# Performance work log

Hardware: AMD Instinct MI355X
Metric: run time of the kernel (lower is better)

Reference implementation:

```python
import jax, jax.numpy as jnp
import numpy as np

TAU = 24            # highpass cutoff period (init kwarg tau)
B, L, D = 16, 4096, 512


def _butter_hp2(tau):
    """2nd-order Butterworth highpass biquad via bilinear transform.
    Matches scipy.signal.iirfilter(2, 1/tau, btype='highpass', output='sos',
    ftype='butter', fs=2.0): one SOS section.
    Returns b: [1,3] numerator taps, A: [1,2,2] companion matrix
    [[-a1,-a2],[1,0]] exactly as built in IIRDecompositionLayer.__init__."""
    K = np.tan(np.pi / (2.0 * tau))  # tan(pi*Wn/2), Wn = 1/tau (Nyquist=1)
    norm = 1.0 / (1.0 + np.sqrt(2.0) * K + K * K)
    b = np.array([norm, -2.0 * norm, norm], dtype=np.float32)
    a1 = 2.0 * (K * K - 1.0) * norm
    a2 = (1.0 - np.sqrt(2.0) * K + K * K) * norm
    A = np.array([[-a1, -a2], [1.0, 0.0]], dtype=np.float32)
    return b[None, :], A[None, :, :]


def setup_inputs() -> dict:
    key = jax.random.key(0)
    x = jax.random.normal(key, (B, L, D), dtype=jnp.float32)
    b, A = _butter_hp2(TAU)
    return {"x": x, "b_coef": jnp.asarray(b), "a_mat": jnp.asarray(A)}


def _combine(c_prev, c_next):
    # composition of affine maps s -> A s + u (linear recurrence)
    A1, u1 = c_prev
    A2, u2 = c_next
    return (jnp.matmul(A2, A1), jnp.einsum('lsn,lbnd->lbsd', A2, u1) + u2)


def _section_pass(x, b3, A, reverse):
    # x: [B,L,D]; b3: [3]; A: [2,2]
    Lx = x.shape[1]
    if reverse:
        # anti-causal taps with 'edge' padding: x[min(t+i, L-1)]
        x1 = jnp.concatenate([x[:, 1:], x[:, -1:]], axis=1)
        x2 = jnp.concatenate([x[:, 2:], x[:, -1:], x[:, -1:]], axis=1)
    else:
        # causal taps with 'edge' padding: x[max(t-i, 0)]
        x1 = jnp.concatenate([x[:, :1], x[:, :-1]], axis=1)
        x2 = jnp.concatenate([x[:, :1], x[:, :1], x[:, :-2]], axis=1)
    bx = b3[0] * x + b3[1] * x1 + b3[2] * x2          # [B,L,D]
    u = jnp.stack([bx, jnp.zeros_like(bx)], axis=2)   # [B,L,2,D] state drive
    u = jnp.transpose(u, (1, 0, 2, 3))                # [L,B,2,D]
    # 'edge' initial state: s_init = [bx_edge, bx_edge], folded into u at the
    # first scanned element (index 0 forward, L-1 reverse)
    idx = Lx - 1 if reverse else 0
    c = bx[:, idx]                                    # [B,D]
    carry = jnp.stack([c, c], axis=1)                 # [B,2,D]
    u = u.at[idx].add(jnp.einsum('sn,bnd->bsd', A, carry))
    As = jnp.broadcast_to(A, (Lx, 2, 2))
    _, res = jax.lax.associative_scan(_combine, (As, u), reverse=reverse)
    return jnp.transpose(res[:, :, 0, :], (1, 0, 2))  # output = state[0] -> [B,L,D]


def reference(x, b_coef, a_mat):
    y = x
    n_sections = b_coef.shape[0]
    for s in range(n_sections):            # small fixed cascade
        for rev in (False, True):          # filtfilt: forward then backward
            y = _section_pass(y, b_coef[s], a_mat[s], rev)
    seasonality = y
    trend = x - seasonality
    return (seasonality, trend)
```

## Files before the change

kernel.cpp:

```cpp
#include <hip/hip_runtime.h>

#define B_   16
#define L_   4096
#define D_   512
#define C_   32
#define NC_  128
#define LOG2C_ 5


__device__ __forceinline__ void pow_M(float A00, float A01,
                                      float& m00, float& m01,
                                      float& m10, float& m11) {
  m00 = A00; m01 = A01; m10 = 1.f; m11 = 0.f;
#pragma unroll
  for (int it = 0; it < LOG2C_; ++it) {
    float n00 = m00 * m00 + m01 * m10;
    float n01 = m00 * m01 + m01 * m11;
    float n10 = m10 * m00 + m11 * m10;
    float n11 = m10 * m01 + m11 * m11;
    m00 = n00; m01 = n01; m10 = n10; m11 = n11;
  }
}

__global__ __launch_bounds__(256) void k_fwd_part(const float* __restrict__ x,
                                                  const float* __restrict__ bc,
                                                  const float* __restrict__ am,
                                                  float* __restrict__ p) {
  int g = blockIdx.x * 256 + threadIdx.x;
  int d = g % D_;
  int i = (g / D_) % NC_;
  int b = g / (D_ * NC_);
  float b0 = bc[0], b1 = bc[1], b2 = bc[2];
  float A00 = am[0], A01 = am[1];
  const float* xb = x + (size_t)b * L_ * D_ + d;
  int l0 = i * C_;
  float xm1, xm2;
  if (i == 0) {
    xm1 = xm2 = xb[0];
  } else {
    xm1 = xb[(size_t)(l0 - 1) * D_];
    xm2 = xb[(size_t)(l0 - 2) * D_];
  }
  float y1 = 0.f, y2 = 0.f;
#pragma unroll
  for (int t = 0; t < C_; ++t) {
    float cur = xb[(size_t)(l0 + t) * D_];
    float bx = b0 * cur + b1 * xm1 + b2 * xm2;
    float y = bx + A00 * y1 + A01 * y2;
    xm2 = xm1; xm1 = cur;
    y2 = y1; y1 = y;
  }
  float* pp = p + (size_t)(b * NC_ + i) * 2 * D_ + d;
  pp[0]  = y1;
  pp[D_] = y2;
}

__global__ __launch_bounds__(256) void k_fwd_scan(const float* __restrict__ x,
                                                  const float* __restrict__ bc,
                                                  const float* __restrict__ am,
                                                  const float* __restrict__ p,
                                                  float* __restrict__ sf) {
  int g = blockIdx.x * 256 + threadIdx.x;
  int d = g % D_;
  int b = g / D_;
  float b0 = bc[0], b1 = bc[1], b2 = bc[2];
  float A00 = am[0], A01 = am[1];
  float m00, m01, m10, m11;
  pow_M(A00, A01, m00, m01, m10, m11);

  float x0 = x[(size_t)b * L_ * D_ + d];
  float bx0 = (b0 + b1 + b2) * x0;
  float s0 = bx0, s1 = bx0;
  const float* pp = p + (size_t)b * NC_ * 2 * D_ + d;
  float* sfp = sf + (size_t)b * (NC_ + 1) * 2 * D_ + d;
  sfp[0] = s0;
  sfp[D_] = s1;
  for (int i = 0; i < NC_; ++i) {
    float p0 = pp[(size_t)i * 2 * D_];
    float p1 = pp[(size_t)i * 2 * D_ + D_];
    float n0 = m00 * s0 + m01 * s1 + p0;
    float n1 = m10 * s0 + m11 * s1 + p1;
    s0 = n0; s1 = n1;
    sfp[(size_t)(i + 1) * 2 * D_]      = s0;
    sfp[(size_t)(i + 1) * 2 * D_ + D_] = s1;
  }
}

__global__ __launch_bounds__(256) void k_bwd_part(const float* __restrict__ x,
                                                  const float* __restrict__ bc,
                                                  const float* __restrict__ am,
                                                  const float* __restrict__ sf,
                                                  float* __restrict__ q) {
  int g = blockIdx.x * 256 + threadIdx.x;
  int d = g % D_;
  int i = (g / D_) % NC_;
  int b = g / (D_ * NC_);
  float b0 = bc[0], b1 = bc[1], b2 = bc[2];
  float A00 = am[0], A01 = am[1];
  const float* xb = x + (size_t)b * L_ * D_ + d;
  const float* sfp = sf + (size_t)b * (NC_ + 1) * 2 * D_ + (size_t)i * 2 * D_ + d;
  float y1 = sfp[0];
  float y2 = sfp[D_];
  int l0 = i * C_;
  float xm1, xm2;
  if (i == 0) {
    xm1 = xm2 = xb[0];
  } else {
    xm1 = xb[(size_t)(l0 - 1) * D_];
    xm2 = xb[(size_t)(l0 - 2) * D_];
  }
  float f[C_];
#pragma unroll
  for (int t = 0; t < C_; ++t) {
    float cur = xb[(size_t)(l0 + t) * D_];
    float bx = b0 * cur + b1 * xm1 + b2 * xm2;
    float y = bx + A00 * y1 + A01 * y2;
    f[t] = y;
    xm2 = xm1; xm1 = cur;
    y2 = y1; y1 = y;
  }
  float fe0, fe1;
  if (i < NC_ - 1) {
    float cur = xb[(size_t)(l0 + C_) * D_];
    float bx = b0 * cur + b1 * xm1 + b2 * xm2;
    fe0 = bx + A00 * y1 + A01 * y2;
    xm2 = xm1; xm1 = cur; y2 = y1; y1 = fe0;
    cur = xb[(size_t)(l0 + C_ + 1) * D_];
    bx = b0 * cur + b1 * xm1 + b2 * xm2;
    fe1 = bx + A00 * y1 + A01 * y2;
  } else {
    fe0 = f[C_ - 1];
    fe1 = f[C_ - 1];
  }
  float z1 = 0.f, z2 = 0.f;
#pragma unroll
  for (int t = C_ - 1; t >= 0; --t) {
    float fp1 = (t == C_ - 1) ? fe0 : f[t + 1];
    float fp2 = (t == C_ - 1) ? fe1 : ((t == C_ - 2) ? fe0 : f[t + 2]);
    float bxb = b0 * f[t] + b1 * fp1 + b2 * fp2;
    float z = bxb + A00 * z1 + A01 * z2;
    z2 = z1; z1 = z;
  }
  float* qp = q + (size_t)(b * NC_ + i) * 2 * D_ + d;
  qp[0]  = z1;
  qp[D_] = z2;
}

__global__ __launch_bounds__(256) void k_bwd_scan(const float* __restrict__ bc,
                                                  const float* __restrict__ am,
                                                  const float* __restrict__ sf,
                                                  const float* __restrict__ q,
                                                  float* __restrict__ sb) {
  int g = blockIdx.x * 256 + threadIdx.x;
  int d = g % D_;
  int b = g / D_;
  float b0 = bc[0], b1 = bc[1], b2 = bc[2];
  float A00 = am[0], A01 = am[1];
  float m00, m01, m10, m11;
  pow_M(A00, A01, m00, m01, m10, m11);

  float fL1 = sf[(size_t)b * (NC_ + 1) * 2 * D_ + (size_t)NC_ * 2 * D_ + d];
  float c = (b0 + b1 + b2) * fL1;
  float s0 = c, s1 = c;
  const float* qp = q + (size_t)b * NC_ * 2 * D_ + d;
  float* sbp = sb + (size_t)b * NC_ * 2 * D_ + d;
  sbp[(size_t)(NC_ - 1) * 2 * D_]      = s0;
  sbp[(size_t)(NC_ - 1) * 2 * D_ + D_] = s1;
  for (int i = NC_ - 1; i >= 1; --i) {
    float q0 = qp[(size_t)i * 2 * D_];
    float q1 = qp[(size_t)i * 2 * D_ + D_];
    float n0 = m00 * s0 + m01 * s1 + q0;
    float n1 = m10 * s0 + m11 * s1 + q1;
    s0 = n0; s1 = n1;
    sbp[(size_t)(i - 1) * 2 * D_]      = s0;
    sbp[(size_t)(i - 1) * 2 * D_ + D_] = s1;
  }
}

__global__ __launch_bounds__(256) void k_final(const float* __restrict__ x,
                                               const float* __restrict__ bc,
                                               const float* __restrict__ am,
                                               const float* __restrict__ sf,
                                               const float* __restrict__ sb,
                                               float* __restrict__ seas,
                                               float* __restrict__ trend) {
  int g = blockIdx.x * 256 + threadIdx.x;
  int d = g % D_;
  int i = (g / D_) % NC_;
  int b = g / (D_ * NC_);
  float b0 = bc[0], b1 = bc[1], b2 = bc[2];
  float A00 = am[0], A01 = am[1];
  const float* xb = x + (size_t)b * L_ * D_ + d;
  const float* sfp = sf + (size_t)b * (NC_ + 1) * 2 * D_ + (size_t)i * 2 * D_ + d;
  float y1 = sfp[0];
  float y2 = sfp[D_];
  int l0 = i * C_;
  float xm1, xm2;
  if (i == 0) {
    xm1 = xm2 = xb[0];
  } else {
    xm1 = xb[(size_t)(l0 - 1) * D_];
    xm2 = xb[(size_t)(l0 - 2) * D_];
  }
  float f[C_];
  float xa[C_];
#pragma unroll
  for (int t = 0; t < C_; ++t) {
    float cur = xb[(size_t)(l0 + t) * D_];
    xa[t] = cur;
    float bx = b0 * cur + b1 * xm1 + b2 * xm2;
    float y = bx + A00 * y1 + A01 * y2;
    f[t] = y;
    xm2 = xm1; xm1 = cur;
    y2 = y1; y1 = y;
  }
  float fe0, fe1;
  if (i < NC_ - 1) {
    float cur = xb[(size_t)(l0 + C_) * D_];
    float bx = b0 * cur + b1 * xm1 + b2 * xm2;
    fe0 = bx + A00 * y1 + A01 * y2;
    xm2 = xm1; xm1 = cur; y2 = y1; y1 = fe0;
    cur = xb[(size_t)(l0 + C_ + 1) * D_];
    bx = b0 * cur + b1 * xm1 + b2 * xm2;
    fe1 = bx + A00 * y1 + A01 * y2;
  } else {
    fe0 = f[C_ - 1];
    fe1 = f[C_ - 1];
  }
  const float* sbp = sb + (size_t)b * NC_ * 2 * D_ + (size_t)i * 2 * D_ + d;
  float z1 = sbp[0];
  float z2 = sbp[D_];
  float* sp = seas + (size_t)b * L_ * D_ + d;
  float* tp = trend + (size_t)b * L_ * D_ + d;
#pragma unroll
  for (int t = C_ - 1; t >= 0; --t) {
    float fp1 = (t == C_ - 1) ? fe0 : f[t + 1];
    float fp2 = (t == C_ - 1) ? fe1 : ((t == C_ - 2) ? fe0 : f[t + 2]);
    float bxb = b0 * f[t] + b1 * fp1 + b2 * fp2;
    float yb = bxb + A00 * z1 + A01 * z2;
    size_t o = (size_t)(l0 + t) * D_;
    __builtin_nontemporal_store(yb, sp + o);
    __builtin_nontemporal_store(xa[t] - yb, tp + o);
    z2 = z1; z1 = yb;
  }
}

extern "C" void kernel_launch(void* const* d_in, const int* in_sizes, int n_in,
                              void* d_out, int out_size, void* d_ws, size_t ws_size,
                              hipStream_t stream) {
  const float* x  = (const float*)d_in[0];
  const float* bc = (const float*)d_in[1];
  const float* am = (const float*)d_in[2];
  float* out = (float*)d_out;
  float* seas  = out;
  float* trend = out + (size_t)B_ * L_ * D_;

  float* ws = (float*)d_ws;
  size_t PN  = (size_t)B_ * NC_ * 2 * D_;
  size_t SFN = (size_t)B_ * (NC_ + 1) * 2 * D_;
  float* p  = ws;
  float* sf = p + PN;
  float* q  = sf + SFN;
  float* sb = q + PN;

  dim3 blk(256);
  int big_grid   = B_ * NC_ * D_ / 256;
  int small_grid = B_ * D_ / 256;

  k_fwd_part<<<big_grid, blk, 0, stream>>>(x, bc, am, p);
  k_fwd_scan<<<small_grid, blk, 0, stream>>>(x, bc, am, p, sf);
  k_bwd_part<<<big_grid, blk, 0, stream>>>(x, bc, am, sf, q);
  k_bwd_scan<<<small_grid, blk, 0, stream>>>(bc, am, sf, q, sb);
  k_final<<<big_grid, blk, 0, stream>>>(x, bc, am, sf, sb, seas, trend);
}
```

Measured before the change: 426.1 us.

## Replace chunked affine scan with overlapped warm-up chunks and materialized forward pass

Drops the exact two-level scan (partial, carry-scan and final kernels) in favour of large 256-step chunks. Each chunk starts from a zero state and runs a 192-step warm-up over the preceding samples, relying on the decay of the stable filter's impulse response. The forward output is written to workspace once and the backward kernel reads it and emits both outputs, so the forward recurrence is no longer recomputed. In exchange it adds warm-up reads and compute, gives fewer threads, and the result is only approximate, bounded by the filter's transient decay.

```diff
diff --git a/kernel.cpp b/kernel.cpp
--- a/kernel.cpp
+++ b/kernel.cpp
@@ -3,245 +3,190 @@
 #define B_   16
 #define L_   4096
 #define D_   512
-#define C_   32
-#define NC_  128
-#define LOG2C_ 5
-
-
-__device__ __forceinline__ void pow_M(float A00, float A01,
-                                      float& m00, float& m01,
-                                      float& m10, float& m11) {
-  m00 = A00; m01 = A01; m10 = 1.f; m11 = 0.f;
-#pragma unroll
-  for (int it = 0; it < LOG2C_; ++it) {
-    float n00 = m00 * m00 + m01 * m10;
-    float n01 = m00 * m01 + m01 * m11;
-    float n10 = m10 * m00 + m11 * m10;
-    float n11 = m10 * m01 + m11 * m11;
-    m00 = n00; m01 = n01; m10 = n10; m11 = n11;
-  }
-}
-
-__global__ __launch_bounds__(256) void k_fwd_part(const float* __restrict__ x,
-                                                  const float* __restrict__ bc,
-                                                  const float* __restrict__ am,
-                                                  float* __restrict__ p) {
+#define C_   256
+#define H_   192
+#define NC_  16
+
+#define SZ_ ((size_t)B_ * L_ * D_)
+
+static_assert(NC_ * C_ == L_, "chunking must tile L");
+static_assert((H_ / 8) % 2 == 0 && (C_ / 8) % 2 == 0, "double-buffer pairing");
+
+
+__global__ __launch_bounds__(256) void k_fwd(const float* __restrict__ x,
+                                             const float* __restrict__ bc,
+                                             const float* __restrict__ am,
+                                             float* __restrict__ f) {
   int g = blockIdx.x * 256 + threadIdx.x;
-  int d = g % D_;
-  int i = (g / D_) % NC_;
-  int b = g / (D_ * NC_);
+  int d = g & (D_ - 1);
+  int ci = (g >> 9) & (NC_ - 1);
+  int b = g >> 13;
   float b0 = bc[0], b1 = bc[1], b2 = bc[2];
   float A00 = am[0], A01 = am[1];
-  const float* xb = x + (size_t)b * L_ * D_ + d;
-  int l0 = i * C_;
-  float xm1, xm2;
-  if (i == 0) {
-    xm1 = xm2 = xb[0];
+  const float* xp = x + (size_t)b * L_ * D_ + d;
+  float* fo = f + (size_t)b * L_ * D_ + d;
+  int l0 = ci * C_;
+
+  float xm1, xm2, y1, y2;
+  float va[8], vb[8], fv[8];
+
+#define LD8(dst, tb)                                               \
+  _Pragma("unroll") for (int u = 0; u < 8; ++u)                    \
+      (dst)[u] = xp[(size_t)((tb) + u) * D_];
+
+#define STEP8(src)                                                 \
+  _Pragma("unroll") for (int u = 0; u < 8; ++u) {                  \
+    float bx = b0 * (src)[u] + b1 * xm1 + b2 * xm2;                \
+    float yy = bx + A00 * y1 + A01 * y2;                           \
+    xm2 = xm1; xm1 = (src)[u]; y2 = y1; y1 = yy;                   \
+    fv[u] = yy;                                                    \
+  }
+
+#define ST8(tb)                                                    \
+  _Pragma("unroll") for (int u = 0; u < 8; ++u)                    \
+      fo[(size_t)((tb) + u) * D_] = fv[u];
+
+  if (ci == 0) {
+    float x0 = xp[0];
+    xm1 = x0; xm2 = x0;
+    float bx0 = (b0 + b1 + b2) * x0;
+    y1 = bx0; y2 = bx0;
   } else {
-    xm1 = xb[(size_t)(l0 - 1) * D_];
-    xm2 = xb[(size_t)(l0 - 2) * D_];
-  }
-  float y1 = 0.f, y2 = 0.f;
-#pragma unroll
-  for (int t = 0; t < C_; ++t) {
-    float cur = xb[(size_t)(l0 + t) * D_];
-    float bx = b0 * cur + b1 * xm1 + b2 * xm2;
-    float y = bx + A00 * y1 + A01 * y2;
-    xm2 = xm1; xm1 = cur;
-    y2 = y1; y1 = y;
-  }
-  float* pp = p + (size_t)(b * NC_ + i) * 2 * D_ + d;
-  pp[0]  = y1;
-  pp[D_] = y2;
-}
-
-__global__ __launch_bounds__(256) void k_fwd_scan(const float* __restrict__ x,
-                                                  const float* __restrict__ bc,
-                                                  const float* __restrict__ am,
-                                                  const float* __restrict__ p,
-                                                  float* __restrict__ sf) {
+    const int ls = l0 - H_;
+    xm1 = xp[(size_t)(ls - 1) * D_];
+    xm2 = xp[(size_t)(ls - 2) * D_];
+    y1 = 0.f; y2 = 0.f;
+    LD8(va, ls);
+#pragma unroll 1
+    for (int gg = 0; gg < H_ / 8; gg += 2) {
+      LD8(vb, ls + (gg + 1) * 8);
+      STEP8(va);
+      if (gg + 2 < H_ / 8) LD8(va, ls + (gg + 2) * 8);
+      STEP8(vb);
+    }
+  }
+  LD8(va, l0);
+#pragma unroll 1
+  for (int gg = 0; gg < C_ / 8; gg += 2) {
+    LD8(vb, l0 + (gg + 1) * 8);
+    STEP8(va);
+    ST8(l0 + gg * 8);
+    if (gg + 2 < C_ / 8) LD8(va, l0 + (gg + 2) * 8);
+    STEP8(vb);
+    ST8(l0 + (gg + 1) * 8);
+  }
+#undef LD8
+#undef STEP8
+#undef ST8
+}
+
+template <bool FUSED>
+__global__ __launch_bounds__(256) void k_bwd(const float* __restrict__ x,
+                                             const float* __restrict__ bc,
+                                             const float* __restrict__ am,
+                                             const float* __restrict__ f,
+                                             float* __restrict__ o0,
+                                             float* __restrict__ o1) {
   int g = blockIdx.x * 256 + threadIdx.x;
-  int d = g % D_;
-  int b = g / D_;
+  int d = g & (D_ - 1);
+  int ci = (g >> 9) & (NC_ - 1);
+  int b = g >> 13;
   float b0 = bc[0], b1 = bc[1], b2 = bc[2];
   float A00 = am[0], A01 = am[1];
-  float m00, m01, m10, m11;
-  pow_M(A00, A01, m00, m01, m10, m11);
-
-  float x0 = x[(size_t)b * L_ * D_ + d];
-  float bx0 = (b0 + b1 + b2) * x0;
-  float s0 = bx0, s1 = bx0;
-  const float* pp = p + (size_t)b * NC_ * 2 * D_ + d;
-  float* sfp = sf + (size_t)b * (NC_ + 1) * 2 * D_ + d;
-  sfp[0] = s0;
-  sfp[D_] = s1;
-  for (int i = 0; i < NC_; ++i) {
-    float p0 = pp[(size_t)i * 2 * D_];
-    float p1 = pp[(size_t)i * 2 * D_ + D_];
-    float n0 = m00 * s0 + m01 * s1 + p0;
-    float n1 = m10 * s0 + m11 * s1 + p1;
-    s0 = n0; s1 = n1;
-    sfp[(size_t)(i + 1) * 2 * D_]      = s0;
-    sfp[(size_t)(i + 1) * 2 * D_ + D_] = s1;
-  }
-}
-
-__global__ __launch_bounds__(256) void k_bwd_part(const float* __restrict__ x,
-                                                  const float* __restrict__ bc,
-                                                  const float* __restrict__ am,
-                                                  const float* __restrict__ sf,
-                                                  float* __restrict__ q) {
-  int g = blockIdx.x * 256 + threadIdx.x;
-  int d = g % D_;
-  int i = (g / D_) % NC_;
-  int b = g / (D_ * NC_);
-  float b0 = bc[0], b1 = bc[1], b2 = bc[2];
-  float A00 = am[0], A01 = am[1];
-  const float* xb = x + (size_t)b * L_ * D_ + d;
-  const float* sfp = sf + (size_t)b * (NC_ + 1) * 2 * D_ + (size_t)i * 2 * D_ + d;
-  float y1 = sfp[0];
-  float y2 = sfp[D_];
-  int l0 = i * C_;
-  float xm1, xm2;
-  if (i == 0) {
-    xm1 = xm2 = xb[0];
+  const float* fi = f + (size_t)b * L_ * D_ + d;
+  const float* xp = x + (size_t)b * L_ * D_ + d;
+  float* s0p = o0 + (size_t)b * L_ * D_ + d;
+  float* s1p = FUSED ? (o1 + (size_t)b * L_ * D_ + d) : o0;
+  int l0 = ci * C_;
+
+  float fp1, fp2, z1, z2;
+  float va[8], vb[8], xa[8], xc[8], zv[8];
+
+#define LD8R(dst, tb)                                              \
+  _Pragma("unroll") for (int u = 0; u < 8; ++u)                    \
+      (dst)[u] = fi[(size_t)((tb) - u) * D_];
+
+#define LD8XR(dst, tb)                                             \
+  _Pragma("unroll") for (int u = 0; u < 8; ++u)                    \
+      (dst)[u] = xp[(size_t)((tb) - u) * D_];
+
+#define STEP8R(src)                                                \
+  _Pragma("unroll") for (int u = 0; u < 8; ++u) {                  \
+    float bx = b0 * (src)[u] + b1 * fp1 + b2 * fp2;                \
+    float zz = bx + A00 * z1 + A01 * z2;                           \
+    fp2 = fp1; fp1 = (src)[u]; z2 = z1; z1 = zz;                   \
+    zv[u] = zz;                                                    \
+  }
+
+#define ST8R(tb, xsrc)                                             \
+  _Pragma("unroll") for (int u = 0; u < 8; ++u) {                  \
+    size_t o = (size_t)((tb) - u) * D_;                            \
+    if (FUSED) {                                                   \
+      __builtin_nontemporal_store(zv[u], s0p + o);                 \
+      __builtin_nontemporal_store((xsrc)[u] - zv[u], s1p + o);     \
+    } else {                                                       \
+      s0p[o] = zv[u];                                              \
+    }                                                              \
+  }
+
+  if (ci == NC_ - 1) {
+    float fl = fi[(size_t)(L_ - 1) * D_];
+    fp1 = fl; fp2 = fl;
+    float c = (b0 + b1 + b2) * fl;
+    z1 = c; z2 = c;
   } else {
-    xm1 = xb[(size_t)(l0 - 1) * D_];
-    xm2 = xb[(size_t)(l0 - 2) * D_];
-  }
-  float f[C_];
-#pragma unroll
-  for (int t = 0; t < C_; ++t) {
-    float cur = xb[(size_t)(l0 + t) * D_];
-    float bx = b0 * cur + b1 * xm1 + b2 * xm2;
-    float y = bx + A00 * y1 + A01 * y2;
-    f[t] = y;
-    xm2 = xm1; xm1 = cur;
-    y2 = y1; y1 = y;
-  }
-  float fe0, fe1;
-  if (i < NC_ - 1) {
-    float cur = xb[(size_t)(l0 + C_) * D_];
-    float bx = b0 * cur + b1 * xm1 + b2 * xm2;
-    fe0 = bx + A00 * y1 + A01 * y2;
-    xm2 = xm1; xm1 = cur; y2 = y1; y1 = fe0;
-    cur = xb[(size_t)(l0 + C_ + 1) * D_];
-    bx = b0 * cur + b1 * xm1 + b2 * xm2;
-    fe1 = bx + A00 * y1 + A01 * y2;
-  } else {
-    fe0 = f[C_ - 1];
-    fe1 = f[C_ - 1];
-  }
-  float z1 = 0.f, z2 = 0.f;
-#pragma unroll
-  for (int t = C_ - 1; t >= 0; --t) {
-    float fp1 = (t == C_ - 1) ? fe0 : f[t + 1];
-    float fp2 = (t == C_ - 1) ? fe1 : ((t == C_ - 2) ? fe0 : f[t + 2]);
-    float bxb = b0 * f[t] + b1 * fp1 + b2 * fp2;
-    float z = bxb + A00 * z1 + A01 * z2;
-    z2 = z1; z1 = z;
-  }
-  float* qp = q + (size_t)(b * NC_ + i) * 2 * D_ + d;
-  qp[0]  = z1;
-  qp[D_] = z2;
-}
-
-__global__ __launch_bounds__(256) void k_bwd_scan(const float* __restrict__ bc,
-                                                  const float* __restrict__ am,
-                                                  const float* __restrict__ sf,
-                                                  const float* __restrict__ q,
-                                                  float* __restrict__ sb) {
-  int g = blockIdx.x * 256 + threadIdx.x;
-  int d = g % D_;
-  int b = g / D_;
-  float b0 = bc[0], b1 = bc[1], b2 = bc[2];
-  float A00 = am[0], A01 = am[1];
-  float m00, m01, m10, m11;
-  pow_M(A00, A01, m00, m01, m10, m11);
-
-  float fL1 = sf[(size_t)b * (NC_ + 1) * 2 * D_ + (size_t)NC_ * 2 * D_ + d];
-  float c = (b0 + b1 + b2) * fL1;
-  float s0 = c, s1 = c;
-  const float* qp = q + (size_t)b * NC_ * 2 * D_ + d;
-  float* sbp = sb + (size_t)b * NC_ * 2 * D_ + d;
-  sbp[(size_t)(NC_ - 1) * 2 * D_]      = s0;
-  sbp[(size_t)(NC_ - 1) * 2 * D_ + D_] = s1;
-  for (int i = NC_ - 1; i >= 1; --i) {
-    float q0 = qp[(size_t)i * 2 * D_];
-    float q1 = qp[(size_t)i * 2 * D_ + D_];
-    float n0 = m00 * s0 + m01 * s1 + q0;
-    float n1 = m10 * s0 + m11 * s1 + q1;
-    s0 = n0; s1 = n1;
-    sbp[(size_t)(i - 1) * 2 * D_]      = s0;
-    sbp[(size_t)(i - 1) * 2 * D_ + D_] = s1;
-  }
-}
-
-__global__ __launch_bounds__(256) void k_final(const float* __restrict__ x,
-                                               const float* __restrict__ bc,
-                                               const float* __restrict__ am,
-                                               const float* __restrict__ sf,
-                                               const float* __restrict__ sb,
+    const int hs = l0 + C_ - 1 + H_;
+    fp1 = fi[(size_t)(hs + 1) * D_];
+    fp2 = fi[(size_t)(hs + 2) * D_];
+    z1 = 0.f; z2 = 0.f;
+    LD8R(va, hs);
+#pragma unroll 1
+    for (int gg = 0; gg < H_ / 8; gg += 2) {
+      LD8R(vb, hs - (gg + 1) * 8);
+      STEP8R(va);
+      if (gg + 2 < H_ / 8) LD8R(va, hs - (gg + 2) * 8);
+      STEP8R(vb);
+    }
+  }
+  const int ts = l0 + C_ - 1;
+  LD8R(va, ts);
+  if (FUSED) LD8XR(xa, ts);
+#pragma unroll 1
+  for (int gg = 0; gg < C_ / 8; gg += 2) {
+    LD8R(vb, ts - (gg + 1) * 8);
+    if (FUSED) LD8XR(xc, ts - (gg + 1) * 8);
+    STEP8R(va);
+    ST8R(ts - gg * 8, xa);
+    if (gg + 2 < C_ / 8) {
+      LD8R(va, ts - (gg + 2) * 8);
+      if (FUSED) LD8XR(xa, ts - (gg + 2) * 8);
+    }
+    STEP8R(vb);
+    ST8R(ts - (gg + 1) * 8, xc);
+  }
+#undef LD8R
+#undef LD8XR
+#undef STEP8R
+#undef ST8R
+}
+
+__global__ __launch_bounds__(256) void k_split(const float* __restrict__ x,
                                                float* __restrict__ seas,
                                                float* __restrict__ trend) {
-  int g = blockIdx.x * 256 + threadIdx.x;
-  int d = g % D_;
-  int i = (g / D_) % NC_;
-  int b = g / (D_ * NC_);
-  float b0 = bc[0], b1 = bc[1], b2 = bc[2];
-  float A00 = am[0], A01 = am[1];
-  const float* xb = x + (size_t)b * L_ * D_ + d;
-  const float* sfp = sf + (size_t)b * (NC_ + 1) * 2 * D_ + (size_t)i * 2 * D_ + d;
-  float y1 = sfp[0];
-  float y2 = sfp[D_];
-  int l0 = i * C_;
-  float xm1, xm2;
-  if (i == 0) {
-    xm1 = xm2 = xb[0];
-  } else {
-    xm1 = xb[(size_t)(l0 - 1) * D_];
-    xm2 = xb[(size_t)(l0 - 2) * D_];
-  }
-  float f[C_];
-  float xa[C_];
-#pragma unroll
-  for (int t = 0; t < C_; ++t) {
-    float cur = xb[(size_t)(l0 + t) * D_];
-    xa[t] = cur;
-    float bx = b0 * cur + b1 * xm1 + b2 * xm2;
-    float y = bx + A00 * y1 + A01 * y2;
-    f[t] = y;
-    xm2 = xm1; xm1 = cur;
-    y2 = y1; y1 = y;
-  }
-  float fe0, fe1;
-  if (i < NC_ - 1) {
-    float cur = xb[(size_t)(l0 + C_) * D_];
-    float bx = b0 * cur + b1 * xm1 + b2 * xm2;
-    fe0 = bx + A00 * y1 + A01 * y2;
-    xm2 = xm1; xm1 = cur; y2 = y1; y1 = fe0;
-    cur = xb[(size_t)(l0 + C_ + 1) * D_];
-    bx = b0 * cur + b1 * xm1 + b2 * xm2;
-    fe1 = bx + A00 * y1 + A01 * y2;
-  } else {
-    fe0 = f[C_ - 1];
-    fe1 = f[C_ - 1];
-  }
-  const float* sbp = sb + (size_t)b * NC_ * 2 * D_ + (size_t)i * 2 * D_ + d;
-  float z1 = sbp[0];
-  float z2 = sbp[D_];
-  float* sp = seas + (size_t)b * L_ * D_ + d;
-  float* tp = trend + (size_t)b * L_ * D_ + d;
-#pragma unroll
-  for (int t = C_ - 1; t >= 0; --t) {
-    float fp1 = (t == C_ - 1) ? fe0 : f[t + 1];
-    float fp2 = (t == C_ - 1) ? fe1 : ((t == C_ - 2) ? fe0 : f[t + 2]);
-    float bxb = b0 * f[t] + b1 * fp1 + b2 * fp2;
-    float yb = bxb + A00 * z1 + A01 * z2;
-    size_t o = (size_t)(l0 + t) * D_;
-    __builtin_nontemporal_store(yb, sp + o);
-    __builtin_nontemporal_store(xa[t] - yb, tp + o);
-    z2 = z1; z1 = yb;
+  size_t n4 = SZ_ / 4;
+  size_t idx = (size_t)blockIdx.x * 256 + threadIdx.x;
+  size_t stride = (size_t)gridDim.x * 256;
+  const float4* x4 = (const float4*)x;
+  float4* s4 = (float4*)seas;
+  float4* t4 = (float4*)trend;
+  for (size_t k = idx; k < n4; k += stride) {
+    float4 zv = t4[k];
+    float4 xv = x4[k];
+    float4 tv;
+    tv.x = xv.x - zv.x; tv.y = xv.y - zv.y;
+    tv.z = xv.z - zv.z; tv.w = xv.w - zv.w;
+    s4[k] = zv;
+    t4[k] = tv;
   }
 }
 
@@ -251,25 +196,20 @@
   const float* x  = (const float*)d_in[0];
   const float* bc = (const float*)d_in[1];
   const float* am = (const float*)d_in[2];
-  float* out = (float*)d_out;
-  float* seas  = out;
-  float* trend = out + (size_t)B_ * L_ * D_;
-
-  float* ws = (float*)d_ws;
-  size_t PN  = (size_t)B_ * NC_ * 2 * D_;
-  size_t SFN = (size_t)B_ * (NC_ + 1) * 2 * D_;
-  float* p  = ws;
-  float* sf = p + PN;
-  float* q  = sf + SFN;
-  float* sb = q + PN;
+  float* outp  = (float*)d_out;
+  float* seas  = outp;
+  float* trend = outp + SZ_;
 
   dim3 blk(256);
-  int big_grid   = B_ * NC_ * D_ / 256;
-  int small_grid = B_ * D_ / 256;
-
-  k_fwd_part<<<big_grid, blk, 0, stream>>>(x, bc, am, p);
-  k_fwd_scan<<<small_grid, blk, 0, stream>>>(x, bc, am, p, sf);
-  k_bwd_part<<<big_grid, blk, 0, stream>>>(x, bc, am, sf, q);
-  k_bwd_scan<<<small_grid, blk, 0, stream>>>(bc, am, sf, q, sb);
-  k_final<<<big_grid, blk, 0, stream>>>(x, bc, am, sf, sb, seas, trend);
-}
+  int grid = (int)(B_ * NC_ * D_ / 256);
+
+  if (ws_size >= SZ_ * sizeof(float)) {
+    float* f = (float*)d_ws;
+    k_fwd<<<grid, blk, 0, stream>>>(x, bc, am, f);
+    k_bwd<true><<<grid, blk, 0, stream>>>(x, bc, am, f, seas, trend);
+  } else {
+    k_fwd<<<grid, blk, 0, stream>>>(x, bc, am, seas);
+    k_bwd<false><<<grid, blk, 0, stream>>>(x, bc, am, seas, trend, nullptr);
+    k_split<<<2048, blk, 0, stream>>>(x, seas, trend);
+  }
+}
```

After: 439.0 us. +3.0%, slower.
